# Kernel optimization log

Hardware: AMD Instinct MI355X
Metric: run time of the kernel (lower is better)

Reference implementation:

```python
import jax, jax.numpy as jnp
import numpy as np

SEQ, B, IN, H, OUT = 600, 4096, 6, 30, 61


def setup_inputs() -> dict:
    key = jax.random.key(0)
    ks = jax.random.split(key, 9)
    s_ih = 1.0 / np.sqrt(H)
    return {
        "X": jax.random.normal(ks[0], (SEQ, B, IN), dtype=jnp.float32),
        "W_ih": jax.random.uniform(ks[1], (4 * H, IN), jnp.float32, -s_ih, s_ih),
        "W_hh": jax.random.uniform(ks[2], (4 * H, H), jnp.float32, -s_ih, s_ih),
        "b_ih": jax.random.uniform(ks[3], (4 * H,), jnp.float32, -s_ih, s_ih),
        "b_hh": jax.random.uniform(ks[4], (4 * H,), jnp.float32, -s_ih, s_ih),
        "W1": jax.random.uniform(ks[5], (H, H), jnp.float32, -s_ih, s_ih),
        "b1": jax.random.uniform(ks[6], (H,), jnp.float32, -s_ih, s_ih),
        "W2": jax.random.uniform(ks[7], (OUT, H), jnp.float32, -s_ih, s_ih),
        "b2": jax.random.uniform(ks[8], (OUT,), jnp.float32, -s_ih, s_ih),
        "batch_size": B,
    }


def _lstm_last_h(X, W_ih, W_hh, b_ih, b_hh):
    # Precompute input projections for all timesteps: [T, B, 4H]
    xg = jnp.einsum("tbi,gi->tbg", X, W_ih) + b_ih + b_hh
    h0 = jnp.zeros((X.shape[1], W_hh.shape[1]), X.dtype)
    c0 = jnp.zeros_like(h0)

    def step(carry, xg_t):
        h, c = carry
        g = xg_t + h @ W_hh.T  # [B, 4H]
        i, f, gg, o = jnp.split(g, 4, axis=-1)  # PyTorch gate order i,f,g,o
        c = jax.nn.sigmoid(f) * c + jax.nn.sigmoid(i) * jnp.tanh(gg)
        h = jax.nn.sigmoid(o) * jnp.tanh(c)
        return (h, c), None

    (h, _), _ = jax.lax.scan(step, (h0, c0), xg)
    return h  # out[-1, :, :]


def reference(X, W_ih, W_hh, b_ih, b_hh, W1, b1, W2, b2, batch_size):
    h = _lstm_last_h(X, W_ih, W_hh, b_ih, b_hh)
    out = h @ W1.T + b1  # fc1
    # dropout(p=0.6) is identity in eval mode
    out = out @ W2.T + b2  # fc2
    return out  # [B, 61]
```

## Files before the change

kernel.cpp:

```cpp
#include <hip/hip_runtime.h>


#define SEQ    600
#define BATCH  4096
#define INP    6
#define HID    30
#define NOUT   61
#define LOG2E  1.4426950408889634f
#define LOG2E2 2.8853900817779268f

typedef __fp16 f16;
typedef f16  f16x2 __attribute__((ext_vector_type(2)));
typedef f16  f16x8 __attribute__((ext_vector_type(8)));
typedef float f32x2 __attribute__((ext_vector_type(2)));
typedef float f32x4 __attribute__((ext_vector_type(4)));

__device__ __forceinline__ float rcp_(float x)  { return __builtin_amdgcn_rcpf(x); }
__device__ __forceinline__ float exp2_(float x) { return __builtin_amdgcn_exp2f(x); }
__device__ __forceinline__ unsigned cvtpk(float a, float b) {
    union { f16x2 h; unsigned u; } c;
    c.h = __builtin_amdgcn_cvt_pkrtz(a, b);
    return c.u;
}
__device__ __forceinline__ f16x8 mk8(unsigned a, unsigned b, unsigned c, unsigned d) {
    union { unsigned u[4]; f16x8 v; } x;
    x.u[0] = a; x.u[1] = b; x.u[2] = c; x.u[3] = d;
    return x.v;
}
__device__ __forceinline__ float sigm_(float x) {
    return rcp_(1.0f + exp2_(-LOG2E * x));
}
__device__ __forceinline__ float tanh_(float x) {
    return fmaf(-2.0f, rcp_(exp2_(LOG2E2 * x) + 1.0f), 1.0f);
}

extern "C" __global__ void __launch_bounds__(64, 1)
lstm_m4(const float* __restrict__ X,   const float* __restrict__ Wih,
        const float* __restrict__ Whh, const float* __restrict__ bih,
        const float* __restrict__ bhh, const float* __restrict__ W1,
        const float* __restrict__ b1,  const float* __restrict__ W2,
        const float* __restrict__ b2,  float* __restrict__ out)
{
    __shared__ __align__(16) float scr[4][136];
    __shared__ float h32[4][32];
    __shared__ float o1s[4][32];

    const int l  = threadIdx.x;
    const int g  = l >> 4;
    const int b  = l & 15;
    const int e0 = blockIdx.x * 4;

    f16x8 Ah[8], Ax[8];
    {
        const int q = b & 3;
        #pragma unroll
        for (int m = 0; m < 8; ++m) {
            const int u  = 4 * m + (b >> 2);
            const bool ov = (u < HID);
            const int row = q * HID + (ov ? u : 0);
            unsigned dh[4], dx[4];
            #pragma unroll
            for (int jp = 0; jp < 4; ++jp) {
                const int k0 = 8 * g + 2 * jp, k1 = k0 + 1;
                float v0 = (ov && k0 < HID) ? Whh[row * HID + k0] : 0.f;
                float v1 = (ov && k1 < HID) ? Whh[row * HID + k1]
                         : ((ov && k1 == 31) ? (bih[row] + bhh[row]) : 0.f);
                dh[jp] = cvtpk(v0, v1);
                float w0 = (ov && k0 < INP) ? Wih[row * INP + k0] : 0.f;
                float w1 = (ov && k1 < INP) ? Wih[row * INP + k1] : 0.f;
                dx[jp] = cvtpk(w0, w1);
            }
            Ah[m] = mk8(dh[0], dh[1], dh[2], dh[3]);
            Ax[m] = mk8(dx[0], dx[1], dx[2], dx[3]);
        }
    }

    const int ad0 = ((16 * b + 4 * g + 0) & 63) * 4;
    const int ad1 = ((16 * b + 4 * g + 1) & 63) * 4;
    const int ad2 = ((16 * b + 4 * g + 2) & 63) * 4;
    const int ad3 = ((16 * b + 4 * g + 3) & 63) * 4;
    const bool isg3 = (g == 3);

    const float* xsrc = X + (size_t)(e0 + (b & 3)) * INP;

    unsigned P = 0;
    float cA = 0.f, cB = 0.f;
    float hA = 0.f, hB = 0.f;

    f32x2 xq0, xq1, xq2;
    { const float* p = xsrc; xq0 = *(const f32x2*)p; xq1 = *(const f32x2*)(p+2); xq2 = *(const f32x2*)(p+4); }

    f32x4 xcA[8], xcB[8];
    const f32x4 ZZ = {0.f, 0.f, 0.f, 0.f};

    #define XACC(DST) do {                                                     \
        const unsigned c0 = cvtpk(xq0.x, xq0.y);                               \
        const unsigned c1 = cvtpk(xq1.x, xq1.y);                               \
        const unsigned c2 = cvtpk(xq2.x, xq2.y);                               \
        const f16x8 Bx = mk8(g == 0 ? c0 : 0u, g == 0 ? c1 : 0u,               \
                             g == 0 ? c2 : 0u, 0u);                            \
        _Pragma("unroll")                                                      \
        for (int m = 0; m < 8; ++m)                                            \
            DST[m] = __builtin_amdgcn_mfma_f32_16x16x32_f16(Ax[m], Bx, ZZ, 0, 0, 0); \
    } while (0)

    XACC(xcA);
    { const float* p = xsrc + (size_t)BATCH * INP;
      xq0 = *(const f32x2*)p; xq1 = *(const f32x2*)(p+2); xq2 = *(const f32x2*)(p+4); }

    #define ITER(XC, XN, T) do {                                               \
                  \
        unsigned d0 = (unsigned)__builtin_amdgcn_ds_bpermute(ad0, (int)P);     \
        unsigned d1 = (unsigned)__builtin_amdgcn_ds_bpermute(ad1, (int)P);     \
        unsigned d2 = (unsigned)__builtin_amdgcn_ds_bpermute(ad2, (int)P);     \
        unsigned d3 = (unsigned)__builtin_amdgcn_ds_bpermute(ad3, (int)P);     \
        d3 = isg3 ? 0x3C000000u : d3;                                          \
        const f16x8 Bh = mk8(d0, d1, d2, d3);                                  \
        f32x4 C[8];                                                            \
        _Pragma("unroll")                                                      \
        for (int m = 0; m < 8; ++m)                                            \
            C[m] = __builtin_amdgcn_mfma_f32_16x16x32_f16(Ah[m], Bh, XC[m], 0, 0, 0); \
        \
        XACC(XN);                                                              \
                                               \
        { int tt = (T) + 2; if (tt > SEQ - 1) tt = SEQ - 1;                    \
          const float* p = xsrc + (size_t)tt * BATCH * INP;                    \
          xq0 = *(const f32x2*)p; xq1 = *(const f32x2*)(p+2);                  \
          xq2 = *(const f32x2*)(p+4); }                                        \
                    \
        if (b < 4) {                                                           \
            _Pragma("unroll")                                                  \
            for (int m = 0; m < 8; ++m)                                        \
                *(f32x4*)&scr[b][(4 * m + g) * 4] = C[m];                      \
        }                                                                      \
                             \
        const f32x4 gA = *(const f32x4*)&scr[g][(2 * b) * 4];                  \
        const f32x4 gB = *(const f32x4*)&scr[g][(2 * b + 1) * 4];              \
                                                \
        const float siA = sigm_(gA.x), sfA = sigm_(gA.y);                      \
        const float tgA = tanh_(gA.z), soA = sigm_(gA.w);                      \
        const float siB = sigm_(gB.x), sfB = sigm_(gB.y);                      \
        const float tgB = tanh_(gB.z), soB = sigm_(gB.w);                      \
        cA = fmaf(sfA, cA, siA * tgA);                                         \
        cB = fmaf(sfB, cB, siB * tgB);                                         \
        hA = soA * tanh_(cA);                                                  \
        hB = soB * tanh_(cB);                                                  \
        P = cvtpk(hA, hB);                                                     \
    } while (0)

    for (int t = 0; t < SEQ; t += 2) {
        ITER(xcA, xcB, t);
        ITER(xcB, xcA, t + 1);
    }
    #undef ITER
    #undef XACC

    if (b < 15) {
        h32[g][2 * b]     = hA;
        h32[g][2 * b + 1] = hB;
    }
    asm volatile("s_waitcnt lgkmcnt(0)" ::: "memory");

    {
        float hr[HID];
        #pragma unroll
        for (int k = 0; k < HID; ++k) hr[k] = h32[g][k];
        float a0 = b1[b];
        const float* w1r0 = W1 + b * HID;
        #pragma unroll
        for (int k = 0; k < HID; ++k) a0 = fmaf(w1r0[k], hr[k], a0);
        o1s[g][b] = a0;
        if (b < 14) {
            float a1 = b1[b + 16];
            const float* w1r1 = W1 + (b + 16) * HID;
            #pragma unroll
            for (int k = 0; k < HID; ++k) a1 = fmaf(w1r1[k], hr[k], a1);
            o1s[g][b + 16] = a1;
        }
    }
    asm volatile("s_waitcnt lgkmcnt(0)" ::: "memory");

    {
        float orr[HID];
        #pragma unroll
        for (int k = 0; k < HID; ++k) orr[k] = o1s[g][k];
        #pragma unroll
        for (int r = 0; r < 4; ++r) {
            const int o = b + 16 * r;
            if (o < NOUT) {
                float a2 = b2[o];
                const float* w2r = W2 + o * HID;
                #pragma unroll
                for (int k = 0; k < HID; ++k) a2 = fmaf(w2r[k], orr[k], a2);
                out[(size_t)(e0 + g) * NOUT + o] = a2;
            }
        }
    }
}

extern "C" void kernel_launch(void* const* d_in, const int* in_sizes, int n_in,
                              void* d_out, int out_size, void* d_ws, size_t ws_size,
                              hipStream_t stream) {
    const float* X   = (const float*)d_in[0];
    const float* Wih = (const float*)d_in[1];
    const float* Whh = (const float*)d_in[2];
    const float* bih = (const float*)d_in[3];
    const float* bhh = (const float*)d_in[4];
    const float* W1  = (const float*)d_in[5];
    const float* b1  = (const float*)d_in[6];
    const float* W2  = (const float*)d_in[7];
    const float* b2  = (const float*)d_in[8];
    float* out = (float*)d_out;

    dim3 grid(BATCH / 4);
    dim3 block(64);
    hipLaunchKernelGGL(lstm_m4, grid, block, 0, stream,
                       X, Wih, Whh, bih, bhh, W1, b1, W2, b2, out);
}
```

Measured before the change: 316.3 us.

## Remove LDS gate transpose by selecting MFMA outputs in registers and remapping hidden layout

Each lane now selects its gate vectors directly from its own MFMA accumulator registers with predicated selects, instead of storing the gate tiles to shared memory and reading them back each timestep. The hidden-unit-to-lane mapping is changed to match the MFMA output layout. The h broadcast is rebuilt to fit it, using eight fp32 bpermutes plus packing where four packed-fp16 bpermutes were used before. This removes LDS stores and loads plus their wait from the recurrent critical path, but doubles the number of permute operations per step and adds select instructions.

After: 370.8 us. +17.2%, slower.

```diff
diff --git a/kernel.cpp b/kernel.cpp
--- a/kernel.cpp
+++ b/kernel.cpp
@@ -27,6 +27,12 @@
     x.u[0] = a; x.u[1] = b; x.u[2] = c; x.u[3] = d;
     return x.v;
 }
+__device__ __forceinline__ float asf(int u) {
+    union { int i; float f; } c; c.i = u; return c.f;
+}
+__device__ __forceinline__ int asi(float f) {
+    union { float f; int i; } c; c.f = f; return c.i;
+}
 __device__ __forceinline__ float sigm_(float x) {
     return rcp_(1.0f + exp2_(-LOG2E * x));
 }
@@ -35,27 +41,31 @@
 }
 
 extern "C" __global__ void __launch_bounds__(64, 1)
-lstm_m4(const float* __restrict__ X,   const float* __restrict__ Wih,
+lstm_m5(const float* __restrict__ X,   const float* __restrict__ Wih,
         const float* __restrict__ Whh, const float* __restrict__ bih,
         const float* __restrict__ bhh, const float* __restrict__ W1,
         const float* __restrict__ b1,  const float* __restrict__ W2,
         const float* __restrict__ b2,  float* __restrict__ out)
 {
-    __shared__ __align__(16) float scr[4][136];
     __shared__ float h32[4][32];
     __shared__ float o1s[4][32];
 
     const int l  = threadIdx.x;
     const int g  = l >> 4;
-    const int b  = l & 15;
+    const int n  = l & 15;
+    const int e  = n & 3;
+    const int j  = n >> 2;
     const int e0 = blockIdx.x * 4;
+    const bool jb0 = (j & 1) != 0;
+    const bool jb1 = (j & 2) != 0;
+    const bool isg3 = (g == 3);
 
     f16x8 Ah[8], Ax[8];
     {
-        const int q = b & 3;
+        const int q = n & 3;
         #pragma unroll
         for (int m = 0; m < 8; ++m) {
-            const int u  = 4 * m + (b >> 2);
+            const int u  = 4 * m + (n >> 2);
             const bool ov = (u < HID);
             const int row = q * HID + (ov ? u : 0);
             unsigned dh[4], dx[4];
@@ -75,15 +85,13 @@
         }
     }
 
-    const int ad0 = ((16 * b + 4 * g + 0) & 63) * 4;
-    const int ad1 = ((16 * b + 4 * g + 1) & 63) * 4;
-    const int ad2 = ((16 * b + 4 * g + 2) & 63) * 4;
-    const int ad3 = ((16 * b + 4 * g + 3) & 63) * 4;
-    const bool isg3 = (g == 3);
-
-    const float* xsrc = X + (size_t)(e0 + (b & 3)) * INP;
-
-    unsigned P = 0;
+    const int A0 = (4 * g + e) * 4;
+    const int A1 = (16 + 4 * g + e) * 4;
+    const int A2 = (32 + 4 * g + e) * 4;
+    const int A3 = (48 + 4 * g + e) * 4;
+
+    const float* xsrc = X + (size_t)(e0 + e) * INP;
+
     float cA = 0.f, cB = 0.f;
     float hA = 0.f, hB = 0.f;
 
@@ -109,13 +117,21 @@
       xq0 = *(const f32x2*)p; xq1 = *(const f32x2*)(p+2); xq2 = *(const f32x2*)(p+4); }
 
     #define ITER(XC, XN, T) do {                                               \
-                  \
-        unsigned d0 = (unsigned)__builtin_amdgcn_ds_bpermute(ad0, (int)P);     \
-        unsigned d1 = (unsigned)__builtin_amdgcn_ds_bpermute(ad1, (int)P);     \
-        unsigned d2 = (unsigned)__builtin_amdgcn_ds_bpermute(ad2, (int)P);     \
-        unsigned d3 = (unsigned)__builtin_amdgcn_ds_bpermute(ad3, (int)P);     \
-        d3 = isg3 ? 0x3C000000u : d3;                                          \
-        const f16x8 Bh = mk8(d0, d1, d2, d3);                                  \
+                         \
+        const int r0 = __builtin_amdgcn_ds_bpermute(A0, asi(hA));              \
+        const int r1 = __builtin_amdgcn_ds_bpermute(A1, asi(hA));              \
+        const int r2 = __builtin_amdgcn_ds_bpermute(A2, asi(hA));              \
+        const int r3 = __builtin_amdgcn_ds_bpermute(A3, asi(hA));              \
+        const int r4 = __builtin_amdgcn_ds_bpermute(A0, asi(hB));              \
+        const int r5 = __builtin_amdgcn_ds_bpermute(A1, asi(hB));              \
+        const int r6 = __builtin_amdgcn_ds_bpermute(A2, asi(hB));              \
+        const int r7 = __builtin_amdgcn_ds_bpermute(A3, asi(hB));              \
+        const unsigned dw0 = cvtpk(asf(r0), asf(r1));                          \
+        const unsigned dw1 = cvtpk(asf(r2), asf(r3));                          \
+        const unsigned dw2 = cvtpk(asf(r4), asf(r5));                          \
+        unsigned dw3 = cvtpk(asf(r6), asf(r7));                                \
+        dw3 = isg3 ? 0x3C000000u : dw3;        \
+        const f16x8 Bh = mk8(dw0, dw1, dw2, dw3);                              \
         f32x4 C[8];                                                            \
         _Pragma("unroll")                                                      \
         for (int m = 0; m < 8; ++m)                                            \
@@ -127,25 +143,22 @@
           const float* p = xsrc + (size_t)tt * BATCH * INP;                    \
           xq0 = *(const f32x2*)p; xq1 = *(const f32x2*)(p+2);                  \
           xq2 = *(const f32x2*)(p+4); }                                        \
-                    \
-        if (b < 4) {                                                           \
-            _Pragma("unroll")                                                  \
-            for (int m = 0; m < 8; ++m)                                        \
-                *(f32x4*)&scr[b][(4 * m + g) * 4] = C[m];                      \
-        }                                                                      \
-                             \
-        const f32x4 gA = *(const f32x4*)&scr[g][(2 * b) * 4];                  \
-        const f32x4 gB = *(const f32x4*)&scr[g][(2 * b + 1) * 4];              \
+                \
+        const f32x4 sA0 = jb0 ? C[2] : C[0];                                   \
+        const f32x4 sA1 = jb0 ? C[6] : C[4];                                   \
+        const f32x4 GA  = jb1 ? sA1 : sA0;                                     \
+        const f32x4 sB0 = jb0 ? C[3] : C[1];                                   \
+        const f32x4 sB1 = jb0 ? C[7] : C[5];                                   \
+        const f32x4 GB  = jb1 ? sB1 : sB0;                                     \
                                                 \
-        const float siA = sigm_(gA.x), sfA = sigm_(gA.y);                      \
-        const float tgA = tanh_(gA.z), soA = sigm_(gA.w);                      \
-        const float siB = sigm_(gB.x), sfB = sigm_(gB.y);                      \
-        const float tgB = tanh_(gB.z), soB = sigm_(gB.w);                      \
+        const float siA = sigm_(GA.x), sfA = sigm_(GA.y);                      \
+        const float tgA = tanh_(GA.z), soA = sigm_(GA.w);                      \
+        const float siB = sigm_(GB.x), sfB = sigm_(GB.y);                      \
+        const float tgB = tanh_(GB.z), soB = sigm_(GB.w);                      \
         cA = fmaf(sfA, cA, siA * tgA);                                         \
         cB = fmaf(sfB, cB, siB * tgB);                                         \
         hA = soA * tanh_(cA);                                                  \
         hB = soB * tanh_(cB);                                                  \
-        P = cvtpk(hA, hB);                                                     \
     } while (0)
 
     for (int t = 0; t < SEQ; t += 2) {
@@ -155,27 +168,25 @@
     #undef ITER
     #undef XACC
 
-    if (b < 15) {
-        h32[g][2 * b]     = hA;
-        h32[g][2 * b + 1] = hB;
-    }
+    h32[e][8 * j + g]     = hA;
+    h32[e][8 * j + 4 + g] = hB;
     asm volatile("s_waitcnt lgkmcnt(0)" ::: "memory");
 
     {
         float hr[HID];
         #pragma unroll
         for (int k = 0; k < HID; ++k) hr[k] = h32[g][k];
-        float a0 = b1[b];
-        const float* w1r0 = W1 + b * HID;
+        float a0 = b1[n];
+        const float* w1r0 = W1 + n * HID;
         #pragma unroll
         for (int k = 0; k < HID; ++k) a0 = fmaf(w1r0[k], hr[k], a0);
-        o1s[g][b] = a0;
-        if (b < 14) {
-            float a1 = b1[b + 16];
-            const float* w1r1 = W1 + (b + 16) * HID;
+        o1s[g][n] = a0;
+        if (n < 14) {
+            float a1 = b1[n + 16];
+            const float* w1r1 = W1 + (n + 16) * HID;
             #pragma unroll
             for (int k = 0; k < HID; ++k) a1 = fmaf(w1r1[k], hr[k], a1);
-            o1s[g][b + 16] = a1;
+            o1s[g][n + 16] = a1;
         }
     }
     asm volatile("s_waitcnt lgkmcnt(0)" ::: "memory");
@@ -186,7 +197,7 @@
         for (int k = 0; k < HID; ++k) orr[k] = o1s[g][k];
         #pragma unroll
         for (int r = 0; r < 4; ++r) {
-            const int o = b + 16 * r;
+            const int o = n + 16 * r;
             if (o < NOUT) {
                 float a2 = b2[o];
                 const float* w2r = W2 + o * HID;
@@ -214,6 +225,6 @@
 
     dim3 grid(BATCH / 4);
     dim3 block(64);
-    hipLaunchKernelGGL(lstm_m4, grid, block, 0, stream,
+    hipLaunchKernelGGL(lstm_m5, grid, block, 0, stream,
                        X, Wih, Whh, bih, bhh, W1, b1, W2, b2, out);
 }
```
